# Kernel optimization log

Hardware: AMD Instinct MI355X
Metric: run time of the kernel (lower is better)

## Reference

```python
import jax, jax.numpy as jnp
import numpy as np

LOG2PI = float(np.log(2.0 * np.pi))
Q_LOGVAR = float(np.log(0.25))  # log(0.5^2)


def _kld(mu, logvar, q_mu, q_logvar):
    return -0.5 * (1.0 + logvar - q_logvar
                   - (jnp.square(mu - q_mu) + jnp.exp(logvar)) / jnp.exp(q_logvar))


def _log_normal(x):
    return -0.5 * (LOG2PI + jnp.square(x))


def setup_inputs() -> dict:
    key = jax.random.key(0)
    ks = jax.random.split(key, 10)
    N, D, E = 8192, 64, 262144
    return {
        "z_mu_n": jax.random.normal(ks[0], (N, D), jnp.float32),
        "z_logvar_n": jax.random.normal(ks[1], (N, D), jnp.float32),
        "z_mu_e": jax.random.normal(ks[2], (N, D), jnp.float32),
        "z_logvar_e": jax.random.normal(ks[3], (N, D), jnp.float32),
        "Alpha_mu": jax.random.normal(ks[4], (D,), jnp.float32),
        "Beta_mu": jax.random.normal(ks[5], (D,), jnp.float32),
        "edge_logits": jax.random.normal(ks[6], (N, N), jnp.float32),
        "mu_Alpha": jax.random.normal(ks[7], (D,), jnp.float32),
        "mu_Beta": jax.random.normal(ks[8], (D,), jnp.float32),
        "edge_index": jax.random.randint(ks[9], (2, E), 0, N, jnp.int64),
        "num_nodes": N,
    }


def reference(z_mu_n, z_logvar_n, z_mu_e, z_logvar_e, Alpha_mu, Beta_mu,
              edge_logits, mu_Alpha, mu_Beta, edge_index, num_nodes):
    N = num_nodes
    i, j = edge_index[0], edge_index[1]
    # single fused symmetric scatter replacing the per-edge Python loop
    adj = jnp.zeros((N, N), jnp.float32).at[i, j].set(1.0).at[j, i].set(1.0)

    # BCEWithLogitsLoss (mean reduction), numerically stable
    x = edge_logits
    logpx_z = jnp.mean(jnp.maximum(x, 0.0) - x * adj + jnp.log1p(jnp.exp(-jnp.abs(x))))

    Alpha_logvar = jnp.full_like(Alpha_mu, Q_LOGVAR)
    Beta_logvar = jnp.full_like(Beta_mu, Q_LOGVAR)

    log_pmu_Alpha = jnp.mean(_log_normal(mu_Alpha))
    log_pmu_Beta = jnp.mean(_log_normal(mu_Beta))

    extra_kl_Alpha = jnp.mean(_kld(mu_Alpha, Alpha_logvar, Alpha_mu, Alpha_logvar))
    extra_kl_Beta = jnp.mean(_kld(mu_Beta, Beta_logvar, Beta_mu, Beta_logvar))

    # [N, D] latents broadcast against [D] prior params
    kl_structure = jnp.mean(_kld(z_mu_e, z_logvar_e, mu_Alpha, Q_LOGVAR))
    kl_semantic = jnp.mean(_kld(z_mu_n, z_logvar_n, mu_Beta, Q_LOGVAR))

    return (log_pmu_Alpha + extra_kl_Alpha + log_pmu_Beta + extra_kl_Beta
            + logpx_z + kl_structure + kl_semantic)
```

## Files before the change

### kernel.cpp

```cpp
#include <hip/hip_runtime.h>


static constexpr double D_LOG2PI = 1.8378770664093453;
static constexpr float  KL_C0    = -1.1931471805599453f;

__device__ __forceinline__ void block_reduce_add(double v, double* acc) {
#pragma unroll
  for (int off = 32; off > 0; off >>= 1)
    v += __shfl_down(v, off, 64);
  __shared__ double s[8];
  const int lane = threadIdx.x & 63;
  const int wv   = threadIdx.x >> 6;
  if (lane == 0) s[wv] = v;
  __syncthreads();
  if (threadIdx.x == 0) {
    double t = s[0];
    const int nw = (blockDim.x + 63) >> 6;
    for (int w = 1; w < nw; ++w) t += s[w];
    atomicAdd(acc, t);
  }
}

__global__ __launch_bounds__(64) void k_init(double* __restrict__ accs,
                                             int* __restrict__ flag,
                                             const int* __restrict__ eidx) {
  const int t = threadIdx.x;
  if (t < 8) accs[t] = 0.0;
  const int w = eidx[2 * t + 1];
  const unsigned long long m = __ballot(w == 0);
  if (t == 0) *flag = (m == 0xFFFFFFFFFFFFFFFFull) ? 1 : 0;
}

__global__ __launch_bounds__(256) void k_softplus(const float4* __restrict__ x,
                                                  long long n4,
                                                  double* __restrict__ acc) {
  long long i = (long long)blockIdx.x * blockDim.x + threadIdx.x;
  const long long stride = (long long)gridDim.x * blockDim.x;
  double local = 0.0;
  for (; i < n4; i += stride) {
    const float4 v = x[i];
    float s = fmaxf(v.x, 0.f) + log1pf(__expf(-fabsf(v.x)));
    s += fmaxf(v.y, 0.f) + log1pf(__expf(-fabsf(v.y)));
    s += fmaxf(v.z, 0.f) + log1pf(__expf(-fabsf(v.z)));
    s += fmaxf(v.w, 0.f) + log1pf(__expf(-fabsf(v.w)));
    local += (double)s;
  }
  block_reduce_add(local, acc);
}

__global__ __launch_bounds__(256) void k_edges(const int* __restrict__ eidx,
                                               const float* __restrict__ x,
                                               int N, int E,
                                               const int* __restrict__ flag,
                                               double* __restrict__ acc) {
  const int is64 = *flag;
  const long long t0 = (long long)blockIdx.x * blockDim.x + threadIdx.x;
  const long long stride = (long long)gridDim.x * blockDim.x;
  double local = 0.0;
  for (long long e = t0; e < E; e += stride) {
    int i, j;
    if (is64) {
      i = eidx[2 * e];
      j = eidx[2 * ((long long)E + e)];
    } else {
      i = eidx[e];
      j = eidx[(long long)E + e];
    }
    float v = x[(long long)i * N + j];
    if (i != j) v += x[(long long)j * N + i];
    local += (double)v;
  }
  block_reduce_add(local, acc);
}

__global__ __launch_bounds__(256) void k_kl(const float4* __restrict__ zmu_n,
                                            const float4* __restrict__ zlv_n,
                                            const float4* __restrict__ zmu_e,
                                            const float4* __restrict__ zlv_e,
                                            const float4* __restrict__ muA,
                                            const float4* __restrict__ muB,
                                            long long n4, int d4mask,
                                            double* __restrict__ acc) {
  long long i = (long long)blockIdx.x * blockDim.x + threadIdx.x;
  const long long stride = (long long)gridDim.x * blockDim.x;
  double local = 0.0;
  for (; i < n4; i += stride) {
    const int dv = (int)(i & d4mask);
    const float4 qa = muA[dv];
    const float4 qb = muB[dv];
    const float4 me = zmu_e[i];
    const float4 le = zlv_e[i];
    const float4 mn = zmu_n[i];
    const float4 ln_ = zlv_n[i];
    float s = 0.f;
    {
      float d0 = me.x - qa.x, d1 = me.y - qa.y, d2 = me.z - qa.z, d3 = me.w - qa.w;
      s += KL_C0 - 0.5f * le.x + 2.f * (d0 * d0 + __expf(le.x));
      s += KL_C0 - 0.5f * le.y + 2.f * (d1 * d1 + __expf(le.y));
      s += KL_C0 - 0.5f * le.z + 2.f * (d2 * d2 + __expf(le.z));
      s += KL_C0 - 0.5f * le.w + 2.f * (d3 * d3 + __expf(le.w));
    }
    {
      float d0 = mn.x - qb.x, d1 = mn.y - qb.y, d2 = mn.z - qb.z, d3 = mn.w - qb.w;
      s += KL_C0 - 0.5f * ln_.x + 2.f * (d0 * d0 + __expf(ln_.x));
      s += KL_C0 - 0.5f * ln_.y + 2.f * (d1 * d1 + __expf(ln_.y));
      s += KL_C0 - 0.5f * ln_.z + 2.f * (d2 * d2 + __expf(ln_.z));
      s += KL_C0 - 0.5f * ln_.w + 2.f * (d3 * d3 + __expf(ln_.w));
    }
    local += (double)s;
  }
  block_reduce_add(local, acc);
}

__global__ __launch_bounds__(64) void k_final(const float* __restrict__ Alpha_mu,
                                              const float* __restrict__ Beta_mu,
                                              const float* __restrict__ mu_A,
                                              const float* __restrict__ mu_B,
                                              const double* __restrict__ accs,
                                              float* __restrict__ out,
                                              int D, double invN2, double invND) {
  const int d = threadIdx.x;
  double t = 0.0;
  if (d < D) {
    const double ma = mu_A[d], mb = mu_B[d];
    const double aa = Alpha_mu[d], bb = Beta_mu[d];
    t = -0.5 * (D_LOG2PI + ma * ma) + 2.0 * (ma - aa) * (ma - aa)
      + -0.5 * (D_LOG2PI + mb * mb) + 2.0 * (mb - bb) * (mb - bb);
  }
#pragma unroll
  for (int off = 32; off > 0; off >>= 1)
    t += __shfl_down(t, off, 64);
  if (d == 0) {
    const double r = (accs[0] - accs[1]) * invN2
                   + accs[2] * invND
                   + t / (double)D;
    out[0] = (float)r;
  }
}

extern "C" void kernel_launch(void* const* d_in, const int* in_sizes, int n_in,
                              void* d_out, int out_size, void* d_ws, size_t ws_size,
                              hipStream_t stream) {
  const float* z_mu_n   = (const float*)d_in[0];
  const float* z_lv_n   = (const float*)d_in[1];
  const float* z_mu_e   = (const float*)d_in[2];
  const float* z_lv_e   = (const float*)d_in[3];
  const float* Alpha_mu = (const float*)d_in[4];
  const float* Beta_mu  = (const float*)d_in[5];
  const float* elog     = (const float*)d_in[6];
  const float* mu_A     = (const float*)d_in[7];
  const float* mu_B     = (const float*)d_in[8];
  const int*   eidx     = (const int*)d_in[9];

  const int D = in_sizes[4];
  const int N = in_sizes[0] / D;
  const int E = in_sizes[9] / 2;
  const long long N2 = (long long)N * N;
  const long long ND = (long long)N * D;

  double* accs = (double*)d_ws;
  int* flag = (int*)(accs + 8);
  float* out = (float*)d_out;

  k_init<<<1, 64, 0, stream>>>(accs, flag, eidx);
  k_softplus<<<4096, 256, 0, stream>>>((const float4*)elog, N2 / 4, accs + 0);
  k_edges<<<1024, 256, 0, stream>>>(eidx, elog, N, E, flag, accs + 1);
  k_kl<<<512, 256, 0, stream>>>((const float4*)z_mu_n, (const float4*)z_lv_n,
                                (const float4*)z_mu_e, (const float4*)z_lv_e,
                                (const float4*)mu_A, (const float4*)mu_B,
                                ND / 4, D / 4 - 1, accs + 2);
  k_final<<<1, 64, 0, stream>>>(Alpha_mu, Beta_mu, mu_A, mu_B, accs, out,
                                D, 1.0 / (double)N2, 1.0 / (double)ND);
}
```

Before: 490.4 us.

## Fuse softplus, edge and KL reductions into one launch with fast softplus

Merges the three reduction kernels into a single launch, giving each task its own range of block indices, so launch gaps go away and the phases can overlap. The softplus is rewritten with the hardware exp2 and log intrinsics in place of log1pf/expf. KL gets 256 blocks instead of 512. The fast log(1+t) loses some precision for small t, and blocks from different roles now compete for resources at the same time.

```diff
diff --git a/kernel.cpp b/kernel.cpp
--- a/kernel.cpp
+++ b/kernel.cpp
@@ -21,6 +21,11 @@
   }
 }
 
+__device__ __forceinline__ float softplus_fast(float x) {
+  const float t = __builtin_amdgcn_exp2f(-1.442695041f * fabsf(x));
+  return fmaxf(x, 0.f) + 0.6931471806f * __builtin_amdgcn_logf(1.f + t);
+}
+
 __global__ __launch_bounds__(64) void k_init(double* __restrict__ accs,
                                              int* __restrict__ flag,
                                              const int* __restrict__ eidx) {
@@ -31,85 +36,77 @@
   if (t == 0) *flag = (m == 0xFFFFFFFFFFFFFFFFull) ? 1 : 0;
 }
 
-__global__ __launch_bounds__(256) void k_softplus(const float4* __restrict__ x,
-                                                  long long n4,
-                                                  double* __restrict__ acc) {
-  long long i = (long long)blockIdx.x * blockDim.x + threadIdx.x;
-  const long long stride = (long long)gridDim.x * blockDim.x;
-  double local = 0.0;
-  for (; i < n4; i += stride) {
-    const float4 v = x[i];
-    float s = fmaxf(v.x, 0.f) + log1pf(__expf(-fabsf(v.x)));
-    s += fmaxf(v.y, 0.f) + log1pf(__expf(-fabsf(v.y)));
-    s += fmaxf(v.z, 0.f) + log1pf(__expf(-fabsf(v.z)));
-    s += fmaxf(v.w, 0.f) + log1pf(__expf(-fabsf(v.w)));
-    local += (double)s;
+__global__ __launch_bounds__(256) void k_main(
+    const float4* __restrict__ x4, long long n4,
+    const int* __restrict__ eidx, const float* __restrict__ x, int N, int E,
+    const int* __restrict__ flag,
+    const float4* __restrict__ zmu_n, const float4* __restrict__ zlv_n,
+    const float4* __restrict__ zmu_e, const float4* __restrict__ zlv_e,
+    const float4* __restrict__ muA, const float4* __restrict__ muB,
+    long long nd4, int d4mask,
+    double* __restrict__ accs, int spB, int edB) {
+  const int b = blockIdx.x;
+  if (b < spB) {
+    long long i = (long long)b * blockDim.x + threadIdx.x;
+    const long long stride = (long long)spB * blockDim.x;
+    double local = 0.0;
+    for (; i < n4; i += stride) {
+      const float4 v = x4[i];
+      float s = softplus_fast(v.x) + softplus_fast(v.y)
+              + softplus_fast(v.z) + softplus_fast(v.w);
+      local += (double)s;
+    }
+    block_reduce_add(local, accs + 0);
+  } else if (b < spB + edB) {
+    const int is64 = *flag;
+    const long long t0 = (long long)(b - spB) * blockDim.x + threadIdx.x;
+    const long long stride = (long long)edB * blockDim.x;
+    double local = 0.0;
+    for (long long e = t0; e < E; e += stride) {
+      int i, j;
+      if (is64) {
+        i = eidx[2 * e];
+        j = eidx[2 * ((long long)E + e)];
+      } else {
+        i = eidx[e];
+        j = eidx[(long long)E + e];
+      }
+      float v = x[(long long)i * N + j];
+      if (i != j) v += x[(long long)j * N + i];
+      local += (double)v;
+    }
+    block_reduce_add(local, accs + 1);
+  } else {
+    long long i = (long long)(b - spB - edB) * blockDim.x + threadIdx.x;
+    const long long stride = (long long)(gridDim.x - spB - edB) * blockDim.x;
+    double local = 0.0;
+    for (; i < nd4; i += stride) {
+      const int dv = (int)(i & d4mask);
+      const float4 qa = muA[dv];
+      const float4 qb = muB[dv];
+      const float4 me = zmu_e[i];
+      const float4 le = zlv_e[i];
+      const float4 mn = zmu_n[i];
+      const float4 ln_ = zlv_n[i];
+      float s = 0.f;
+      {
+        float d0 = me.x - qa.x, d1 = me.y - qa.y, d2 = me.z - qa.z, d3 = me.w - qa.w;
+        s += KL_C0 - 0.5f * le.x + 2.f * (d0 * d0 + __expf(le.x));
+        s += KL_C0 - 0.5f * le.y + 2.f * (d1 * d1 + __expf(le.y));
+        s += KL_C0 - 0.5f * le.z + 2.f * (d2 * d2 + __expf(le.z));
+        s += KL_C0 - 0.5f * le.w + 2.f * (d3 * d3 + __expf(le.w));
+      }
+      {
+        float d0 = mn.x - qb.x, d1 = mn.y - qb.y, d2 = mn.z - qb.z, d3 = mn.w - qb.w;
+        s += KL_C0 - 0.5f * ln_.x + 2.f * (d0 * d0 + __expf(ln_.x));
+        s += KL_C0 - 0.5f * ln_.y + 2.f * (d1 * d1 + __expf(ln_.y));
+        s += KL_C0 - 0.5f * ln_.z + 2.f * (d2 * d2 + __expf(ln_.z));
+        s += KL_C0 - 0.5f * ln_.w + 2.f * (d3 * d3 + __expf(ln_.w));
+      }
+      local += (double)s;
+    }
+    block_reduce_add(local, accs + 2);
   }
-  block_reduce_add(local, acc);
-}
-
-__global__ __launch_bounds__(256) void k_edges(const int* __restrict__ eidx,
-                                               const float* __restrict__ x,
-                                               int N, int E,
-                                               const int* __restrict__ flag,
-                                               double* __restrict__ acc) {
-  const int is64 = *flag;
-  const long long t0 = (long long)blockIdx.x * blockDim.x + threadIdx.x;
-  const long long stride = (long long)gridDim.x * blockDim.x;
-  double local = 0.0;
-  for (long long e = t0; e < E; e += stride) {
-    int i, j;
-    if (is64) {
-      i = eidx[2 * e];
-      j = eidx[2 * ((long long)E + e)];
-    } else {
-      i = eidx[e];
-      j = eidx[(long long)E + e];
-    }
-    float v = x[(long long)i * N + j];
-    if (i != j) v += x[(long long)j * N + i];
-    local += (double)v;
-  }
-  block_reduce_add(local, acc);
-}
-
-__global__ __launch_bounds__(256) void k_kl(const float4* __restrict__ zmu_n,
-                                            const float4* __restrict__ zlv_n,
-                                            const float4* __restrict__ zmu_e,
-                                            const float4* __restrict__ zlv_e,
-                                            const float4* __restrict__ muA,
-                                            const float4* __restrict__ muB,
-                                            long long n4, int d4mask,
-                                            double* __restrict__ acc) {
-  long long i = (long long)blockIdx.x * blockDim.x + threadIdx.x;
-  const long long stride = (long long)gridDim.x * blockDim.x;
-  double local = 0.0;
-  for (; i < n4; i += stride) {
-    const int dv = (int)(i & d4mask);
-    const float4 qa = muA[dv];
-    const float4 qb = muB[dv];
-    const float4 me = zmu_e[i];
-    const float4 le = zlv_e[i];
-    const float4 mn = zmu_n[i];
-    const float4 ln_ = zlv_n[i];
-    float s = 0.f;
-    {
-      float d0 = me.x - qa.x, d1 = me.y - qa.y, d2 = me.z - qa.z, d3 = me.w - qa.w;
-      s += KL_C0 - 0.5f * le.x + 2.f * (d0 * d0 + __expf(le.x));
-      s += KL_C0 - 0.5f * le.y + 2.f * (d1 * d1 + __expf(le.y));
-      s += KL_C0 - 0.5f * le.z + 2.f * (d2 * d2 + __expf(le.z));
-      s += KL_C0 - 0.5f * le.w + 2.f * (d3 * d3 + __expf(le.w));
-    }
-    {
-      float d0 = mn.x - qb.x, d1 = mn.y - qb.y, d2 = mn.z - qb.z, d3 = mn.w - qb.w;
-      s += KL_C0 - 0.5f * ln_.x + 2.f * (d0 * d0 + __expf(ln_.x));
-      s += KL_C0 - 0.5f * ln_.y + 2.f * (d1 * d1 + __expf(ln_.y));
-      s += KL_C0 - 0.5f * ln_.z + 2.f * (d2 * d2 + __expf(ln_.z));
-      s += KL_C0 - 0.5f * ln_.w + 2.f * (d3 * d3 + __expf(ln_.w));
-    }
-    local += (double)s;
-  }
-  block_reduce_add(local, acc);
 }
 
 __global__ __launch_bounds__(64) void k_final(const float* __restrict__ Alpha_mu,
@@ -162,13 +159,17 @@
   int* flag = (int*)(accs + 8);
   float* out = (float*)d_out;
 
+  const int spB = 4096, edB = 1024, klB = 256;
+
   k_init<<<1, 64, 0, stream>>>(accs, flag, eidx);
-  k_softplus<<<4096, 256, 0, stream>>>((const float4*)elog, N2 / 4, accs + 0);
-  k_edges<<<1024, 256, 0, stream>>>(eidx, elog, N, E, flag, accs + 1);
-  k_kl<<<512, 256, 0, stream>>>((const float4*)z_mu_n, (const float4*)z_lv_n,
-                                (const float4*)z_mu_e, (const float4*)z_lv_e,
-                                (const float4*)mu_A, (const float4*)mu_B,
-                                ND / 4, D / 4 - 1, accs + 2);
+  k_main<<<spB + edB + klB, 256, 0, stream>>>(
+      (const float4*)elog, N2 / 4,
+      eidx, elog, N, E, flag,
+      (const float4*)z_mu_n, (const float4*)z_lv_n,
+      (const float4*)z_mu_e, (const float4*)z_lv_e,
+      (const float4*)mu_A, (const float4*)mu_B,
+      ND / 4, D / 4 - 1,
+      accs, spB, edB);
   k_final<<<1, 64, 0, stream>>>(Alpha_mu, Beta_mu, mu_A, mu_B, accs, out,
                                 D, 1.0 / (double)N2, 1.0 / (double)ND);
 }
```

Result: faster. 404.4 us (-17.5%).
